# Performance work log

Hardware: AMD Instinct MI355X
Metric: run time of the kernel (lower is better)

## Reference

```python
import jax, jax.numpy as jnp
import numpy as np

TAU = 2.0
V_TH = 1.0
ALPHA = 2.0  # ATan surrogate alpha (spikingjelly default)

@jax.custom_vjp
def atan_heaviside(x):
    # Forward: Heaviside spike; backward: ATan surrogate gradient.
    return (x >= 0).astype(x.dtype)

def _atan_fwd(x):
    return atan_heaviside(x), x

def _atan_bwd(x, g):
    sg = (ALPHA / 2.0) / (1.0 + (jnp.pi / 2.0 * ALPHA * x) ** 2)
    return (g * sg,)

atan_heaviside.defvjp(_atan_fwd, _atan_bwd)

def lif_scan(cur):
    # cur: [T, B, F] input currents. LIF: H = V + (X - V)/tau; S = H >= v_th; hard reset V = H*(1-S).
    def step(v, x_t):
        h = v + (x_t - v) / TAU
        s = atan_heaviside(h - V_TH)
        v_new = h * (1.0 - s)
        return v_new, s
    v0 = jnp.zeros(cur.shape[1:], dtype=cur.dtype)
    _, spikes = jax.lax.scan(step, v0, cur)
    return spikes

def setup_inputs() -> dict:
    key = jax.random.key(0)
    k1, k2 = jax.random.split(key)
    T, B, F_in, F_out = 64, 256, 1024, 1024
    x = jax.random.normal(k1, (T, B, F_in), dtype=jnp.float32)
    W = jax.random.normal(k2, (F_out, F_in), dtype=jnp.float32) * (1.0 / np.sqrt(F_in))
    return {"x": x, "W": W}

def reference(x, W):
    # Linear projection over all timesteps, then multi-step LIF recurrence.
    cur = jnp.einsum('tbf,of->tbo', x, W)  # [T, B, F_out]
    return lif_scan(cur)
```

## Files before the change

kernel.cpp:

```cpp
#include <hip/hip_runtime.h>


#define T_DIM 64
#define B_DIM 256
#define F_DIM 1024
#define K_DIM 1024
#define M_DIM 16384
#define COLS  (B_DIM * F_DIM)
#define KP    2048
#define MARGIN 6e-5f
#define LIST_CAP 32768

typedef __attribute__((ext_vector_type(8))) short short8;
typedef __attribute__((ext_vector_type(4))) float floatx4;

#define ASYNC_CP16(gp, lp)                                                     \
    __builtin_amdgcn_global_load_lds(                                          \
        (const __attribute__((address_space(1))) unsigned int*)(gp),           \
        (__attribute__((address_space(3))) unsigned int*)(lp), 16, 0, 0)

__device__ inline unsigned short f32_to_bf16_rne(float f) {
    unsigned int u = __builtin_bit_cast(unsigned int, f);
    unsigned int r = (u + 0x7FFFu + ((u >> 16) & 1u)) >> 16;
    return (unsigned short)r;
}
__device__ inline float bf16_to_f32(unsigned short h) {
    unsigned int u = ((unsigned int)h) << 16;
    return __builtin_bit_cast(float, u);
}

__global__ __launch_bounds__(256) void split_kernel(
    const float* __restrict__ x, const float* __restrict__ Wm,
    unsigned short* __restrict__ A, unsigned short* __restrict__ B,
    unsigned int* __restrict__ counter)
{
    if (blockIdx.x == 0 && threadIdx.x == 0) *counter = 0;
    const int blk = blockIdx.x;
    const float* in;
    unsigned short* dst;
    int g;
    int orow;
    if (blk < 16384) {
        g = blk * 256 + threadIdx.x;
        int e = g * 4;
        int row = e >> 10;
        orow = ((row & 255) << 6) | (row >> 8);
        in = x; dst = A;
    } else {
        g = (blk - 16384) * 256 + threadIdx.x;
        int e = g * 4;
        orow = e >> 10;
        in = Wm; dst = B;
    }
    int k = (g * 4) & 1023;
    float4 v = reinterpret_cast<const float4*>(in)[g];
    ushort4 h, l;
    float f;
    f = v.x; h.x = f32_to_bf16_rne(f); l.x = f32_to_bf16_rne(f - bf16_to_f32(h.x));
    f = v.y; h.y = f32_to_bf16_rne(f); l.y = f32_to_bf16_rne(f - bf16_to_f32(h.y));
    f = v.z; h.z = f32_to_bf16_rne(f); l.z = f32_to_bf16_rne(f - bf16_to_f32(h.z));
    f = v.w; h.w = f32_to_bf16_rne(f); l.w = f32_to_bf16_rne(f - bf16_to_f32(h.w));
    reinterpret_cast<ushort4*>(dst)[(size_t)orow * (KP / 4) + (k >> 2)] = h;
    reinterpret_cast<ushort4*>(dst)[(size_t)orow * (KP / 4) + 256 + (k >> 2)] = l;
}

__global__ __launch_bounds__(256, 2) void gemm_scan_kernel(
    const unsigned short* __restrict__ A,
    const unsigned short* __restrict__ B,
    float* __restrict__ out,
    unsigned int* __restrict__ counter, unsigned int* __restrict__ list)
{
    __shared__ unsigned short Ah[128 * 32];
    __shared__ unsigned short Al[128 * 32];
    __shared__ unsigned short Bh[256 * 32];
    __shared__ unsigned short Bl[256 * 32];

    const int tid  = threadIdx.x;
    const int lane = tid & 63;
    const int wv   = tid >> 6;
    const int lid = blockIdx.x;
    const int mt  = ((lid & 7) << 4) | (lid >> 5);
    const int nt  = (lid >> 3) & 3;
    const int m0  = mt * 128;
    const int n0  = nt * 256;
    const int wm  = (wv & 1) * 64;
    const int wn  = (wv >> 1) * 128;

    floatx4 acc[4][8] = {};

    const int srow = tid >> 2;
    const int slin = (tid & 3) * 8;
    const int ssw  = (((tid & 3) ^ ((tid >> 3) & 3)) * 8);
    const int lrow = lane & 15;
    const int q    = lane >> 4;
    const int rsw  = (lrow >> 1) & 3;

    const unsigned short* Ab = A + (size_t)m0 * KP;
    const unsigned short* Bb = B + (size_t)n0 * KP;

    for (int k0 = 0; k0 < 1024; k0 += 32) {
        __syncthreads();
        ASYNC_CP16(Ab + (size_t)srow * KP + k0 + ssw,                Ah + srow * 32 + slin);
        ASYNC_CP16(Ab + (size_t)(srow + 64) * KP + k0 + ssw,         Ah + (srow + 64) * 32 + slin);
        ASYNC_CP16(Ab + (size_t)srow * KP + 1024 + k0 + ssw,         Al + srow * 32 + slin);
        ASYNC_CP16(Ab + (size_t)(srow + 64) * KP + 1024 + k0 + ssw,  Al + (srow + 64) * 32 + slin);
        ASYNC_CP16(Bb + (size_t)srow * KP + k0 + ssw,                Bh + srow * 32 + slin);
        ASYNC_CP16(Bb + (size_t)(srow + 64) * KP + k0 + ssw,         Bh + (srow + 64) * 32 + slin);
        ASYNC_CP16(Bb + (size_t)(srow + 128) * KP + k0 + ssw,        Bh + (srow + 128) * 32 + slin);
        ASYNC_CP16(Bb + (size_t)(srow + 192) * KP + k0 + ssw,        Bh + (srow + 192) * 32 + slin);
        ASYNC_CP16(Bb + (size_t)srow * KP + 1024 + k0 + ssw,         Bl + srow * 32 + slin);
        ASYNC_CP16(Bb + (size_t)(srow + 64) * KP + 1024 + k0 + ssw,  Bl + (srow + 64) * 32 + slin);
        ASYNC_CP16(Bb + (size_t)(srow + 128) * KP + 1024 + k0 + ssw, Bl + (srow + 128) * 32 + slin);
        ASYNC_CP16(Bb + (size_t)(srow + 192) * KP + 1024 + k0 + ssw, Bl + (srow + 192) * 32 + slin);
        __syncthreads();

        const int sl = (q ^ rsw) * 8;
        short8 ah[4], al[4];
#pragma unroll
        for (int i = 0; i < 4; ++i) {
            ah[i] = *reinterpret_cast<const short8*>(&Ah[(wm + i * 16 + lrow) * 32 + sl]);
            al[i] = *reinterpret_cast<const short8*>(&Al[(wm + i * 16 + lrow) * 32 + sl]);
        }
#pragma unroll
        for (int jh = 0; jh < 2; ++jh) {
            short8 bh[4], bl[4];
#pragma unroll
            for (int j4 = 0; j4 < 4; ++j4) {
                const int jr = (wn + (jh * 4 + j4) * 16 + lrow) * 32 + sl;
                bh[j4] = *reinterpret_cast<const short8*>(&Bh[jr]);
                bl[j4] = *reinterpret_cast<const short8*>(&Bl[jr]);
            }
#pragma unroll
            for (int i = 0; i < 4; ++i)
#pragma unroll
                for (int j4 = 0; j4 < 4; ++j4)
                    acc[i][jh * 4 + j4] = __builtin_amdgcn_mfma_f32_16x16x32_bf16(
                        ah[i], bh[j4], acc[i][jh * 4 + j4], 0, 0, 0);
#pragma unroll
            for (int i = 0; i < 4; ++i)
#pragma unroll
                for (int j4 = 0; j4 < 4; ++j4)
                    acc[i][jh * 4 + j4] = __builtin_amdgcn_mfma_f32_16x16x32_bf16(
                        al[i], bh[j4], acc[i][jh * 4 + j4], 0, 0, 0);
#pragma unroll
            for (int i = 0; i < 4; ++i)
#pragma unroll
                for (int j4 = 0; j4 < 4; ++j4)
                    acc[i][jh * 4 + j4] = __builtin_amdgcn_mfma_f32_16x16x32_bf16(
                        ah[i], bl[j4], acc[i][jh * 4 + j4], 0, 0, 0);
        }
    }

    const int col = lane & 15;
    const int b_g = mt * 2 + (wv & 1);

    unsigned int fmask = 0;
#pragma unroll
    for (int j = 0; j < 8; ++j) {
        float v = 0.f;
        bool fl = false;
#pragma unroll
        for (int i = 0; i < 4; ++i) {
#pragma unroll
            for (int qq = 0; qq < 4; ++qq) {
                if (q == qq) {
#pragma unroll
                    for (int r = 0; r < 4; ++r) {
                        float cu = acc[i][j][r];
                        float h = v + (cu - v) * 0.5f;
                        float d = h - 1.0f;
                        bool sp = (d >= 0.f);
                        fl |= (fabsf(d) < MARGIN);
                        acc[i][j][r] = sp ? 1.0f : 0.0f;
                        v = sp ? 0.f : h;
                    }
                }
                v = __shfl(v, qq * 16 + col, 64);
            }
        }
        if (fl) fmask |= (1u << j);
    }
    fmask |= __shfl_xor(fmask, 16, 64);
    fmask |= __shfl_xor(fmask, 32, 64);

    float* outp = out + (size_t)b_g * F_DIM;
#pragma unroll
    for (int i = 0; i < 4; ++i)
#pragma unroll
        for (int j = 0; j < 8; ++j)
#pragma unroll
            for (int r = 0; r < 4; ++r) {
                int t = i * 16 + q * 4 + r;
                int o = n0 + wn + j * 16 + col;
                outp[(size_t)t * COLS + o] = acc[i][j][r];
            }

    if (q == 0 && fmask) {
        for (int j = 0; j < 8; ++j)
            if (fmask & (1u << j)) {
                unsigned int idx = atomicAdd(counter, 1u);
                if (idx < LIST_CAP)
                    list[idx] = (unsigned int)((b_g << 10) | (n0 + wn + j * 16 + col));
            }
    }
}

__global__ __launch_bounds__(256) void fixup_kernel(
    const float* __restrict__ x, const float* __restrict__ W,
    const unsigned int* __restrict__ counter, const unsigned int* __restrict__ list,
    float* __restrict__ out)
{
    __shared__ double curd[T_DIM];
    __shared__ float wrow[K_DIM];
    unsigned int n = *counter;
    if (n > LIST_CAP) n = LIST_CAP;
    const int wv = threadIdx.x >> 6, lane = threadIdx.x & 63;

    for (unsigned int idx = blockIdx.x; idx < n; idx += gridDim.x) {
        const unsigned int c = list[idx];
        const int b = c >> 10, o = c & 1023;
        __syncthreads();
        for (int k = threadIdx.x; k < K_DIM; k += 256) wrow[k] = W[(size_t)o * K_DIM + k];
        __syncthreads();
        for (int it = 0; it < 16; ++it) {
            const int t = it * 4 + wv;
            const float* xp = x + (size_t)t * COLS + (size_t)b * F_DIM + lane * 16;
            double s = 0.0;
#pragma unroll
            for (int qq = 0; qq < 4; ++qq) {
                float4 xv = reinterpret_cast<const float4*>(xp)[qq];
                float4 wq = *reinterpret_cast<const float4*>(&wrow[lane * 16 + qq * 4]);
                s += (double)xv.x * (double)wq.x + (double)xv.y * (double)wq.y +
                     (double)xv.z * (double)wq.z + (double)xv.w * (double)wq.w;
            }
#pragma unroll
            for (int off = 32; off > 0; off >>= 1) s += __shfl_down(s, off, 64);
            if (lane == 0) curd[t] = s;
        }
        __syncthreads();
        if (threadIdx.x == 0) {
            double v = 0.0;
            for (int t = 0; t < T_DIM; ++t) {
                double h = v + (curd[t] - v) * 0.5;
                bool s = (h >= 1.0);
                out[(size_t)t * COLS + c] = s ? 1.0f : 0.0f;
                v = s ? 0.0 : h;
            }
        }
        __syncthreads();
    }
}

#define TILE 64
#define KC 32
#define XS_LD 36
#define SC_LD 65

__global__ __launch_bounds__(256) void lif_fused_kernel(
    const float* __restrict__ x, const float* __restrict__ Wm, float* __restrict__ out)
{
    __shared__ __align__(16) unsigned char smem_raw[TILE * SC_LD * sizeof(double)];
    float* sf = reinterpret_cast<float*>(smem_raw);
    double* sd = reinterpret_cast<double*>(smem_raw);
    float* Xs = sf;
    float* Ws = sf + TILE * XS_LD;

    const int b = blockIdx.y;
    const int o0 = blockIdx.x * TILE;
    const int tid = threadIdx.x;
    const int tx = tid & 15, ty = tid >> 4;

    double acc[4][4];
#pragma unroll
    for (int i = 0; i < 4; ++i)
#pragma unroll
        for (int j = 0; j < 4; ++j) acc[i][j] = 0.0;

    const int r = tid >> 3, c4 = (tid & 7) * 4;
    const float* xbase = x + (size_t)b * F_DIM;

    for (int k0 = 0; k0 < K_DIM; k0 += KC) {
        __syncthreads();
        float4 xv0 = *reinterpret_cast<const float4*>(xbase + (size_t)r * COLS + k0 + c4);
        float4 xv1 = *reinterpret_cast<const float4*>(xbase + (size_t)(r + 32) * COLS + k0 + c4);
        *reinterpret_cast<float4*>(Xs + r * XS_LD + c4) = xv0;
        *reinterpret_cast<float4*>(Xs + (r + 32) * XS_LD + c4) = xv1;
        float4 wv0 = *reinterpret_cast<const float4*>(Wm + (size_t)(o0 + r) * K_DIM + k0 + c4);
        float4 wv1 = *reinterpret_cast<const float4*>(Wm + (size_t)(o0 + r + 32) * K_DIM + k0 + c4);
        *reinterpret_cast<float4*>(Ws + r * XS_LD + c4) = wv0;
        *reinterpret_cast<float4*>(Ws + (r + 32) * XS_LD + c4) = wv1;
        __syncthreads();
#pragma unroll 4
        for (int kk = 0; kk < KC; ++kk) {
            double xa[4], wb[4];
#pragma unroll
            for (int i = 0; i < 4; ++i) xa[i] = (double)Xs[(4 * ty + i) * XS_LD + kk];
#pragma unroll
            for (int j = 0; j < 4; ++j) wb[j] = (double)Ws[(4 * tx + j) * XS_LD + kk];
#pragma unroll
            for (int i = 0; i < 4; ++i)
#pragma unroll
                for (int j = 0; j < 4; ++j) acc[i][j] = fma(xa[i], wb[j], acc[i][j]);
        }
    }
    __syncthreads();
#pragma unroll
    for (int i = 0; i < 4; ++i)
#pragma unroll
        for (int j = 0; j < 4; ++j) sd[(4 * ty + i) * SC_LD + (4 * tx + j)] = acc[i][j];
    __syncthreads();
    if (tid < TILE) {
        double v = 0.0;
        float* outp = out + (size_t)b * F_DIM + o0 + tid;
        for (int t = 0; t < T_DIM; ++t) {
            double cu = sd[t * SC_LD + tid];
            double h = v + (cu - v) * 0.5;
            bool s = (h >= 1.0);
            outp[(size_t)t * COLS] = s ? 1.0f : 0.0f;
            v = s ? 0.0 : h;
        }
    }
}

extern "C" void kernel_launch(void* const* d_in, const int* in_sizes, int n_in,
                              void* d_out, int out_size, void* d_ws, size_t ws_size,
                              hipStream_t stream) {
    const float* x = (const float*)d_in[0];
    const float* Wm = (const float*)d_in[1];
    float* out = (float*)d_out;

    const size_t OFF_A   = 0;
    const size_t OFF_B   = OFF_A + (size_t)M_DIM * KP * 2;
    const size_t OFF_CNT = OFF_B + (size_t)F_DIM * KP * 2;
    const size_t OFF_LST = OFF_CNT + 256;
    const size_t NEEDED  = OFF_LST + (size_t)LIST_CAP * 4;

    if (ws_size < NEEDED) {
        dim3 grid(F_DIM / TILE, B_DIM, 1);
        lif_fused_kernel<<<grid, dim3(256), 0, stream>>>(x, Wm, out);
        return;
    }

    unsigned char* ws = (unsigned char*)d_ws;
    unsigned short* Abuf = (unsigned short*)(ws + OFF_A);
    unsigned short* Bbuf = (unsigned short*)(ws + OFF_B);
    unsigned int* counter = (unsigned int*)(ws + OFF_CNT);
    unsigned int* list = (unsigned int*)(ws + OFF_LST);

    split_kernel<<<dim3(16384 + 1024), dim3(256), 0, stream>>>(x, Wm, Abuf, Bbuf, counter);
    gemm_scan_kernel<<<dim3(512), dim3(256), 0, stream>>>(Abuf, Bbuf, out, counter, list);
    fixup_kernel<<<dim3(512), dim3(256), 0, stream>>>(x, Wm, counter, list, out);
}
```

Before: 227.1 us.

## Double-buffer LDS tiles and use 512-thread blocks in split-bf16 GEMM-scan

```diff
diff --git a/kernel.cpp b/kernel.cpp
--- a/kernel.cpp
+++ b/kernel.cpp
@@ -64,16 +64,16 @@
     reinterpret_cast<ushort4*>(dst)[(size_t)orow * (KP / 4) + 256 + (k >> 2)] = l;
 }
 
-__global__ __launch_bounds__(256, 2) void gemm_scan_kernel(
+__global__ __launch_bounds__(512, 2) void gemm_scan_kernel(
     const unsigned short* __restrict__ A,
     const unsigned short* __restrict__ B,
     float* __restrict__ out,
     unsigned int* __restrict__ counter, unsigned int* __restrict__ list)
 {
-    __shared__ unsigned short Ah[128 * 32];
-    __shared__ unsigned short Al[128 * 32];
-    __shared__ unsigned short Bh[256 * 32];
-    __shared__ unsigned short Bl[256 * 32];
+    __shared__ unsigned short Ah0[128 * 32], Al0[128 * 32];
+    __shared__ unsigned short Bh0[256 * 32], Bl0[256 * 32];
+    __shared__ unsigned short Ah1[128 * 32], Al1[128 * 32];
+    __shared__ unsigned short Bh1[256 * 32], Bl1[256 * 32];
 
     const int tid  = threadIdx.x;
     const int lane = tid & 63;
@@ -84,79 +84,102 @@
     const int m0  = mt * 128;
     const int n0  = nt * 256;
     const int wm  = (wv & 1) * 64;
-    const int wn  = (wv >> 1) * 128;
-
-    floatx4 acc[4][8] = {};
+    const int wn  = (wv >> 1) * 64;
+
+    floatx4 acc[4][4] = {};
 
     const int srow = tid >> 2;
     const int slin = (tid & 3) * 8;
-    const int ssw  = (((tid & 3) ^ ((tid >> 3) & 3)) * 8);
+    const int ssw  = (((tid & 3) ^ ((srow >> 1) & 3)) * 8);
     const int lrow = lane & 15;
     const int q    = lane >> 4;
     const int rsw  = (lrow >> 1) & 3;
+    const int sl   = (q ^ rsw) * 8;
 
     const unsigned short* Ab = A + (size_t)m0 * KP;
     const unsigned short* Bb = B + (size_t)n0 * KP;
 
-    for (int k0 = 0; k0 < 1024; k0 += 32) {
-        __syncthreads();
-        ASYNC_CP16(Ab + (size_t)srow * KP + k0 + ssw,                Ah + srow * 32 + slin);
-        ASYNC_CP16(Ab + (size_t)(srow + 64) * KP + k0 + ssw,         Ah + (srow + 64) * 32 + slin);
-        ASYNC_CP16(Ab + (size_t)srow * KP + 1024 + k0 + ssw,         Al + srow * 32 + slin);
-        ASYNC_CP16(Ab + (size_t)(srow + 64) * KP + 1024 + k0 + ssw,  Al + (srow + 64) * 32 + slin);
-        ASYNC_CP16(Bb + (size_t)srow * KP + k0 + ssw,                Bh + srow * 32 + slin);
-        ASYNC_CP16(Bb + (size_t)(srow + 64) * KP + k0 + ssw,         Bh + (srow + 64) * 32 + slin);
-        ASYNC_CP16(Bb + (size_t)(srow + 128) * KP + k0 + ssw,        Bh + (srow + 128) * 32 + slin);
-        ASYNC_CP16(Bb + (size_t)(srow + 192) * KP + k0 + ssw,        Bh + (srow + 192) * 32 + slin);
-        ASYNC_CP16(Bb + (size_t)srow * KP + 1024 + k0 + ssw,         Bl + srow * 32 + slin);
-        ASYNC_CP16(Bb + (size_t)(srow + 64) * KP + 1024 + k0 + ssw,  Bl + (srow + 64) * 32 + slin);
-        ASYNC_CP16(Bb + (size_t)(srow + 128) * KP + 1024 + k0 + ssw, Bl + (srow + 128) * 32 + slin);
-        ASYNC_CP16(Bb + (size_t)(srow + 192) * KP + 1024 + k0 + ssw, Bl + (srow + 192) * 32 + slin);
-        __syncthreads();
-
-        const int sl = (q ^ rsw) * 8;
-        short8 ah[4], al[4];
-#pragma unroll
-        for (int i = 0; i < 4; ++i) {
-            ah[i] = *reinterpret_cast<const short8*>(&Ah[(wm + i * 16 + lrow) * 32 + sl]);
-            al[i] = *reinterpret_cast<const short8*>(&Al[(wm + i * 16 + lrow) * 32 + sl]);
-        }
-#pragma unroll
-        for (int jh = 0; jh < 2; ++jh) {
-            short8 bh[4], bl[4];
-#pragma unroll
-            for (int j4 = 0; j4 < 4; ++j4) {
-                const int jr = (wn + (jh * 4 + j4) * 16 + lrow) * 32 + sl;
-                bh[j4] = *reinterpret_cast<const short8*>(&Bh[jr]);
-                bl[j4] = *reinterpret_cast<const short8*>(&Bl[jr]);
-            }
-#pragma unroll
-            for (int i = 0; i < 4; ++i)
-#pragma unroll
-                for (int j4 = 0; j4 < 4; ++j4)
-                    acc[i][jh * 4 + j4] = __builtin_amdgcn_mfma_f32_16x16x32_bf16(
-                        ah[i], bh[j4], acc[i][jh * 4 + j4], 0, 0, 0);
-#pragma unroll
-            for (int i = 0; i < 4; ++i)
-#pragma unroll
-                for (int j4 = 0; j4 < 4; ++j4)
-                    acc[i][jh * 4 + j4] = __builtin_amdgcn_mfma_f32_16x16x32_bf16(
-                        al[i], bh[j4], acc[i][jh * 4 + j4], 0, 0, 0);
-#pragma unroll
-            for (int i = 0; i < 4; ++i)
-#pragma unroll
-                for (int j4 = 0; j4 < 4; ++j4)
-                    acc[i][jh * 4 + j4] = __builtin_amdgcn_mfma_f32_16x16x32_bf16(
-                        ah[i], bl[j4], acc[i][jh * 4 + j4], 0, 0, 0);
-        }
-    }
+    const unsigned short* ga_h  = Ab + (size_t)srow * KP + ssw;
+    const unsigned short* ga_l  = ga_h + 1024;
+    const unsigned short* gb0_h = Bb + (size_t)srow * KP + ssw;
+    const unsigned short* gb0_l = gb0_h + 1024;
+    const unsigned short* gb1_h = gb0_h + (size_t)128 * KP;
+    const unsigned short* gb1_l = gb1_h + 1024;
+
+    const int ldsA  = srow * 32 + slin;
+    const int ldsB1 = (srow + 128) * 32 + slin;
+
+    int aoff[4], boff[4];
+#pragma unroll
+    for (int i = 0; i < 4; ++i) aoff[i] = (wm + i * 16 + lrow) * 32 + sl;
+#pragma unroll
+    for (int j = 0; j < 4; ++j) boff[j] = (wn + j * 16 + lrow) * 32 + sl;
+
+#define STAGE(AhB, AlB, BhB, BlB, kk) do {                                     \
+        ASYNC_CP16(ga_h + (kk),  &AhB[ldsA]);                                  \
+        ASYNC_CP16(ga_l + (kk),  &AlB[ldsA]);                                  \
+        ASYNC_CP16(gb0_h + (kk), &BhB[ldsA]);                                  \
+        ASYNC_CP16(gb1_h + (kk), &BhB[ldsB1]);                                 \
+        ASYNC_CP16(gb0_l + (kk), &BlB[ldsA]);                                  \
+        ASYNC_CP16(gb1_l + (kk), &BlB[ldsB1]);                                 \
+    } while (0)
+
+#define COMPUTE(AhB, AlB, BhB, BlB) do {                                       \
+        short8 ah[4], al[4], bh[4], bl[4];                                     \
+        _Pragma("unroll")                                                      \
+        for (int i = 0; i < 4; ++i) {                                          \
+            ah[i] = *reinterpret_cast<const short8*>(&AhB[aoff[i]]);           \
+            al[i] = *reinterpret_cast<const short8*>(&AlB[aoff[i]]);           \
+        }                                                                      \
+        _Pragma("unroll")                                                      \
+        for (int j = 0; j < 4; ++j) {                                          \
+            bh[j] = *reinterpret_cast<const short8*>(&BhB[boff[j]]);           \
+            bl[j] = *reinterpret_cast<const short8*>(&BlB[boff[j]]);           \
+        }                                                                      \
+        __builtin_amdgcn_s_setprio(1);                                         \
+        _Pragma("unroll")                                                      \
+        for (int i = 0; i < 4; ++i)                                            \
+            _Pragma("unroll")                                                  \
+            for (int j = 0; j < 4; ++j)                                        \
+                acc[i][j] = __builtin_amdgcn_mfma_f32_16x16x32_bf16(           \
+                    ah[i], bh[j], acc[i][j], 0, 0, 0);                         \
+        _Pragma("unroll")                                                      \
+        for (int i = 0; i < 4; ++i)                                            \
+            _Pragma("unroll")                                                  \
+            for (int j = 0; j < 4; ++j)                                        \
+                acc[i][j] = __builtin_amdgcn_mfma_f32_16x16x32_bf16(           \
+                    al[i], bh[j], acc[i][j], 0, 0, 0);                         \
+        _Pragma("unroll")                                                      \
+        for (int i = 0; i < 4; ++i)                                            \
+            _Pragma("unroll")                                                  \
+            for (int j = 0; j < 4; ++j)                                        \
+                acc[i][j] = __builtin_amdgcn_mfma_f32_16x16x32_bf16(           \
+                    ah[i], bl[j], acc[i][j], 0, 0, 0);                         \
+        __builtin_amdgcn_s_setprio(0);                                         \
+    } while (0)
+
+    STAGE(Ah0, Al0, Bh0, Bl0, 0);
+    __syncthreads();
+
+#pragma unroll 1
+    for (int kt = 0; kt < 32; kt += 2) {
+        STAGE(Ah1, Al1, Bh1, Bl1, (kt + 1) * 32);
+        COMPUTE(Ah0, Al0, Bh0, Bl0);
+        __syncthreads();
+        if (kt + 2 < 32) STAGE(Ah0, Al0, Bh0, Bl0, (kt + 2) * 32);
+        COMPUTE(Ah1, Al1, Bh1, Bl1);
+        __syncthreads();
+    }
+
+#undef STAGE
+#undef COMPUTE
 
     const int col = lane & 15;
     const int b_g = mt * 2 + (wv & 1);
 
     unsigned int fmask = 0;
 #pragma unroll
-    for (int j = 0; j < 8; ++j) {
+    for (int j = 0; j < 4; ++j) {
         float v = 0.f;
         bool fl = false;
 #pragma unroll
@@ -187,7 +210,7 @@
 #pragma unroll
     for (int i = 0; i < 4; ++i)
 #pragma unroll
-        for (int j = 0; j < 8; ++j)
+        for (int j = 0; j < 4; ++j)
 #pragma unroll
             for (int r = 0; r < 4; ++r) {
                 int t = i * 16 + q * 4 + r;
@@ -196,7 +219,7 @@
             }
 
     if (q == 0 && fmask) {
-        for (int j = 0; j < 8; ++j)
+        for (int j = 0; j < 4; ++j)
             if (fmask & (1u << j)) {
                 unsigned int idx = atomicAdd(counter, 1u);
                 if (idx < LIST_CAP)
@@ -348,6 +371,6 @@
     unsigned int* list = (unsigned int*)(ws + OFF_LST);
 
     split_kernel<<<dim3(16384 + 1024), dim3(256), 0, stream>>>(x, Wm, Abuf, Bbuf, counter);
-    gemm_scan_kernel<<<dim3(512), dim3(256), 0, stream>>>(Abuf, Bbuf, out, counter, list);
+    gemm_scan_kernel<<<dim3(512), dim3(512), 0, stream>>>(Abuf, Bbuf, out, counter, list);
     fixup_kernel<<<dim3(512), dim3(256), 0, stream>>>(x, Wm, counter, list, out);
 }
```

Result: no change. 228.8 us (+0.8%).
